# Performance work log

Hardware: AMD Instinct MI355X
Metric: run time of the kernel (lower is better)

Reference implementation:

```python
import jax, jax.numpy as jnp
import numpy as np

N_NODES = 50000
N_EDGES = 800000
D_IN = 64
F1 = 64
F2 = 64
D_HID = 100


def setup_inputs() -> dict:
    key = jax.random.key(0)
    ks = jax.random.split(key, 12)
    x = jax.random.normal(ks[0], (N_NODES, D_IN), dtype=jnp.float32)
    edge_src = jax.random.randint(ks[1], (N_EDGES,), 0, N_NODES, dtype=jnp.int32)
    edge_dst = jax.random.randint(ks[2], (N_EDGES,), 0, N_NODES, dtype=jnp.int32)
    # stands in for pre-normalized GCN adjacency values (D^-1/2 (A+I) D^-1/2)
    edge_weight = jax.random.uniform(ks[3], (N_EDGES,), dtype=jnp.float32)
    def glorot(k, shape):
        lim = np.sqrt(6.0 / (shape[0] + shape[1]))
        return jax.random.uniform(k, shape, jnp.float32, -lim, lim)
    W1 = glorot(ks[4], (D_IN, F1))
    b1 = jnp.zeros((F1,), jnp.float32)
    W2 = glorot(ks[5], (F1, F2))
    b2 = jnp.zeros((F2,), jnp.float32)
    Wd = glorot(ks[6], (F2, D_HID))
    bd = jnp.zeros((D_HID,), jnp.float32)
    Wo = glorot(ks[7], (D_HID, 1))
    bo = jnp.zeros((1,), jnp.float32)
    return {"x": x, "edge_src": edge_src, "edge_dst": edge_dst,
            "edge_weight": edge_weight, "W1": W1, "b1": b1, "W2": W2,
            "b2": b2, "Wd": Wd, "bd": bd, "Wo": Wo, "bo": bo}


def _gcn_conv(x, edge_src, edge_dst, edge_weight, W, b):
    # spektral GCNConv: out = swish(A_norm @ (X @ W) + b)
    h = x @ W                                        # [N, F]
    msg = h[edge_src] * edge_weight[:, None]          # [E, F] gather + scale
    agg = jax.ops.segment_sum(msg, edge_dst, num_segments=N_NODES)  # [N, F]
    return jax.nn.swish(agg + b)


def reference(x, edge_src, edge_dst, edge_weight, W1, b1, W2, b2, Wd, bd, Wo, bo):
    h = _gcn_conv(x, edge_src, edge_dst, edge_weight, W1, b1)
    h = _gcn_conv(h, edge_src, edge_dst, edge_weight, W2, b2)
    h = jax.nn.swish(h @ Wd + bd)                    # Dense(100, swish)
    return jax.nn.sigmoid(h @ Wo + bo)               # Dense(1, sigmoid) -> [N, 1]
```

## Files before the change

kernel.cpp:

```cpp
#include <hip/hip_runtime.h>
#include <hip/hip_fp16.h>

#define N_NODES 50000
#define N_EDGES 800000
#define D 64
#define DHID 100
#define NTILES (N_NODES / 16)
#define NCT 7
#define CAP 64
#define NGROUPS 8
#define NSLICES 390
#define FILL_BLOCKS (NGROUPS * NSLICES)
#define MM_BLOCKS ((NTILES + 3) / 4)
#define DST_PER_GROUP (N_NODES / NGROUPS)
#define FSTRIDE (NSLICES * 256)
#define KMAX 9

typedef unsigned short ushort;
typedef unsigned int uint;
typedef __attribute__((ext_vector_type(8))) short s16x8;
typedef __attribute__((ext_vector_type(4))) float f32x4;

#define MFMA16(A, B, C) __builtin_amdgcn_mfma_f32_16x16x32_bf16((A), (B), (C), 0, 0, 0)

__device__ __forceinline__ float swishf(float x) { return x / (1.0f + __expf(-x)); }

__device__ __forceinline__ ushort f2bf(float f) {
    uint u = __float_as_uint(f);
    uint r = (u + 0x7fffu + ((u >> 16) & 1u)) >> 16;
    return (ushort)r;
}
__device__ __forceinline__ float bf2f(ushort h) { return __uint_as_float((uint)h << 16); }
__device__ __forceinline__ float bf_lo(uint d) { return __uint_as_float(d << 16); }
__device__ __forceinline__ float bf_hi(uint d) { return __uint_as_float(d & 0xffff0000u); }

__device__ __forceinline__ float hwf(uint e) {
    return __half2float(__ushort_as_half((ushort)(e >> 16)));
}

__device__ __forceinline__ void accum8(float* acc, uint4 v, float w) {
    acc[0] = fmaf(w, bf_lo(v.x), acc[0]);
    acc[1] = fmaf(w, bf_hi(v.x), acc[1]);
    acc[2] = fmaf(w, bf_lo(v.y), acc[2]);
    acc[3] = fmaf(w, bf_hi(v.y), acc[3]);
    acc[4] = fmaf(w, bf_lo(v.z), acc[4]);
    acc[5] = fmaf(w, bf_hi(v.z), acc[5]);
    acc[6] = fmaf(w, bf_lo(v.w), acc[6]);
    acc[7] = fmaf(w, bf_hi(v.w), acc[7]);
}

__device__ __forceinline__ void gather_node2(const ushort* __restrict__ H,
                                             const uint* __restrict__ bucket,
                                             const int* __restrict__ degp,
                                             int j, int fg, float* acc) {
#pragma unroll
    for (int t = 0; t < 8; ++t) acc[t] = 0.f;
    const int sA = j * 4, sB = 16 + j * 4;
    uint4 eA = *((const uint4*)(bucket + sA));
    uint4 eB = *((const uint4*)(bucket + sB));
    int degv = min(*degp, CAP);

    bool pA = sA < degv, pB = sB < degv;
    uint4 vA0, vA1, vA2, vA3, vB0, vB1, vB2, vB3;
    float wA0 = 0, wA1 = 0, wA2 = 0, wA3 = 0;
    float wB0 = 0, wB1 = 0, wB2 = 0, wB3 = 0;
    if (pA) {
        wA0 = hwf(eA.x);
        wA1 = (sA + 1 < degv) ? hwf(eA.y) : 0.f;
        wA2 = (sA + 2 < degv) ? hwf(eA.z) : 0.f;
        wA3 = (sA + 3 < degv) ? hwf(eA.w) : 0.f;
        uint i0 = min(eA.x & 0xffffu, (uint)(N_NODES - 1));
        uint i1 = min(eA.y & 0xffffu, (uint)(N_NODES - 1));
        uint i2 = min(eA.z & 0xffffu, (uint)(N_NODES - 1));
        uint i3 = min(eA.w & 0xffffu, (uint)(N_NODES - 1));
        vA0 = *((const uint4*)(H + ((size_t)i0 << 6) + (fg << 3)));
        vA1 = *((const uint4*)(H + ((size_t)i1 << 6) + (fg << 3)));
        vA2 = *((const uint4*)(H + ((size_t)i2 << 6) + (fg << 3)));
        vA3 = *((const uint4*)(H + ((size_t)i3 << 6) + (fg << 3)));
    }
    if (pB) {
        wB0 = hwf(eB.x);
        wB1 = (sB + 1 < degv) ? hwf(eB.y) : 0.f;
        wB2 = (sB + 2 < degv) ? hwf(eB.z) : 0.f;
        wB3 = (sB + 3 < degv) ? hwf(eB.w) : 0.f;
        uint i0 = min(eB.x & 0xffffu, (uint)(N_NODES - 1));
        uint i1 = min(eB.y & 0xffffu, (uint)(N_NODES - 1));
        uint i2 = min(eB.z & 0xffffu, (uint)(N_NODES - 1));
        uint i3 = min(eB.w & 0xffffu, (uint)(N_NODES - 1));
        vB0 = *((const uint4*)(H + ((size_t)i0 << 6) + (fg << 3)));
        vB1 = *((const uint4*)(H + ((size_t)i1 << 6) + (fg << 3)));
        vB2 = *((const uint4*)(H + ((size_t)i2 << 6) + (fg << 3)));
        vB3 = *((const uint4*)(H + ((size_t)i3 << 6) + (fg << 3)));
    }
    if (pA) {
        accum8(acc, vA0, wA0);
        accum8(acc, vA1, wA1);
        accum8(acc, vA2, wA2);
        accum8(acc, vA3, wA3);
    }
    if (pB) {
        accum8(acc, vB0, wB0);
        accum8(acc, vB1, wB1);
        accum8(acc, vB2, wB2);
        accum8(acc, vB3, wB3);
    }
    for (int base = 32; base < degv; base += 16) {
        int s0 = base + j * 4;
        if (s0 < degv) {
            uint4 e = *((const uint4*)(bucket + s0));
            float w0 = hwf(e.x);
            float w1 = (s0 + 1 < degv) ? hwf(e.y) : 0.f;
            float w2 = (s0 + 2 < degv) ? hwf(e.z) : 0.f;
            float w3 = (s0 + 3 < degv) ? hwf(e.w) : 0.f;
            uint s0i = min(e.x & 0xffffu, (uint)(N_NODES - 1));
            uint s1i = min(e.y & 0xffffu, (uint)(N_NODES - 1));
            uint s2i = min(e.z & 0xffffu, (uint)(N_NODES - 1));
            uint s3i = min(e.w & 0xffffu, (uint)(N_NODES - 1));
            uint4 v0 = *((const uint4*)(H + ((size_t)s0i << 6) + (fg << 3)));
            uint4 v1 = *((const uint4*)(H + ((size_t)s1i << 6) + (fg << 3)));
            uint4 v2 = *((const uint4*)(H + ((size_t)s2i << 6) + (fg << 3)));
            uint4 v3 = *((const uint4*)(H + ((size_t)s3i << 6) + (fg << 3)));
            accum8(acc, v0, w0);
            accum8(acc, v1, w1);
            accum8(acc, v2, w2);
            accum8(acc, v3, w3);
        }
    }
#pragma unroll
    for (int t = 0; t < 8; ++t) {
        acc[t] += __shfl_xor(acc[t], 8, 64);
        acc[t] += __shfl_xor(acc[t], 16, 64);
    }
}

__global__ __launch_bounds__(256) void fill_and_l1(const int* __restrict__ src,
                                                   const int* __restrict__ dst,
                                                   const float* __restrict__ w,
                                                   int* __restrict__ deg,
                                                   uint* __restrict__ csr,
                                                   const float* __restrict__ X,
                                                   const float* __restrict__ W,
                                                   const float* __restrict__ W2,
                                                   const float* __restrict__ Wd,
                                                   short* __restrict__ W2T2,
                                                   short* __restrict__ WdT2,
                                                   ushort* __restrict__ H) {
    __shared__ __align__(16) short sBT[2][D][72];
    int tid = threadIdx.x;

    if (blockIdx.x < FILL_BLOCKS) {
        const int g = blockIdx.x & (NGROUPS - 1);
        const int s = blockIdx.x >> 3;
        const int lo = g * DST_PER_GROUP;
        const int e0 = s * 256 + tid;
        int d[KMAX];
        bool mk[KMAX];
#pragma unroll
        for (int k = 0; k < KMAX; ++k) {
            int e = e0 + k * FSTRIDE;
            int dv = (e < N_EDGES) ? __builtin_nontemporal_load(dst + e) : -1;
            d[k] = dv;
            mk[k] = ((uint)(dv - lo) < (uint)DST_PER_GROUP);
        }
        float wv9[KMAX];
        int sv9[KMAX];
#pragma unroll
        for (int k = 0; k < KMAX; ++k)
            if (mk[k]) {
                int e = e0 + k * FSTRIDE;
                wv9[k] = __builtin_nontemporal_load(w + e);
                sv9[k] = __builtin_nontemporal_load(src + e);
            }
        int r9[KMAX];
#pragma unroll
        for (int k = 0; k < KMAX; ++k)
            if (mk[k]) r9[k] = atomicAdd(&deg[d[k]], 1);
#pragma unroll
        for (int k = 0; k < KMAX; ++k)
            if (mk[k]) {
                uint hw = (uint)__half_as_ushort(__float2half_rn(wv9[k]));
                uint payload = (uint)sv9[k] | (hw << 16);
                int r = min(r9[k], CAP - 1);
                csr[(d[k] << 6) + r] = payload;
            }
        return;
    }

    if (blockIdx.x >= FILL_BLOCKS + MM_BLOCKS) {
        if (blockIdx.x == FILL_BLOCKS + MM_BLOCKS) {
            for (int idx = tid; idx < D * D; idx += 256) {
                int k = idx >> 6, c = idx & 63;
                float wv = W2[idx];
                ushort hi = f2bf(wv);
                W2T2[(size_t)c * D + k] = (short)hi;
                W2T2[(size_t)(D + c) * D + k] = (short)f2bf(wv - bf2f(hi));
            }
        } else {
            for (int idx = tid; idx < NCT * 16 * D; idx += 256) {
                int jj = idx >> 6, k = idx & 63;
                float wv = (jj < DHID) ? Wd[k * DHID + jj] : 0.f;
                ushort hi = f2bf(wv);
                WdT2[(size_t)jj * D + k] = (short)hi;
                WdT2[(size_t)(NCT * 16 + jj) * D + k] = (short)f2bf(wv - bf2f(hi));
            }
        }
        return;
    }

    for (int idx = tid; idx < D * D; idx += 256) {
        int k = idx >> 6, c = idx & 63;
        float wv = W[idx];
        ushort hi = f2bf(wv);
        sBT[0][c][k] = (short)hi;
        sBT[1][c][k] = (short)f2bf(wv - bf2f(hi));
    }
    __syncthreads();
    int wv_ = tid >> 6, lane = tid & 63, quad = lane >> 4, m = lane & 15;
    int tile = min((blockIdx.x - FILL_BLOCKS) * 4 + wv_, NTILES - 1);
    int node0 = tile * 16;

    f32x4 acc[4] = {{0,0,0,0},{0,0,0,0},{0,0,0,0},{0,0,0,0}};
#pragma unroll
    for (int kt = 0; kt < 2; ++kt) {
        int k0 = kt * 32 + quad * 8;
        const float* xp = X + ((size_t)(node0 + m) << 6) + k0;
        f32x4 xa = __builtin_nontemporal_load((const f32x4*)xp);
        f32x4 xb = __builtin_nontemporal_load((const f32x4*)(xp + 4));
        float xv[8] = {xa[0], xa[1], xa[2], xa[3], xb[0], xb[1], xb[2], xb[3]};
        s16x8 ahi, alo;
#pragma unroll
        for (int jj = 0; jj < 8; ++jj) {
            ushort hi = f2bf(xv[jj]);
            ahi[jj] = (short)hi;
            alo[jj] = (short)f2bf(xv[jj] - bf2f(hi));
        }
#pragma unroll
        for (int ct = 0; ct < 4; ++ct) {
            int n = ct * 16 + m;
            s16x8 bhi = *((const s16x8*)&sBT[0][n][k0]);
            s16x8 blo = *((const s16x8*)&sBT[1][n][k0]);
            acc[ct] = MFMA16(ahi, bhi, acc[ct]);
            acc[ct] = MFMA16(ahi, blo, acc[ct]);
            acc[ct] = MFMA16(alo, bhi, acc[ct]);
        }
    }
    __syncthreads();
    short (*rep)[16][72] = (short(*)[16][72])&sBT[0][0][0];
#pragma unroll
    for (int ct = 0; ct < 4; ++ct)
#pragma unroll
        for (int r = 0; r < 4; ++r)
            rep[wv_][quad * 4 + r][ct * 16 + m] = (short)f2bf(acc[ct][r]);
#pragma unroll
    for (int half = 0; half < 2; ++half) {
        int r = (lane >> 3) + half * 8;
        int c0 = (lane & 7) * 8;
        s16x8 v = *((const s16x8*)&rep[wv_][r][c0]);
        *((s16x8*)(H + ((size_t)(node0 + r) << 6) + c0)) = v;
    }
}

__global__ __launch_bounds__(256) void gather_act(const ushort* __restrict__ H,
                                                  const int* __restrict__ deg,
                                                  const uint* __restrict__ csr,
                                                  const float* __restrict__ bias,
                                                  ushort* __restrict__ actOut) {
    int tid = threadIdx.x;
    int wave = tid >> 6, lane = tid & 63;
    int h = lane >> 5, j = (lane >> 3) & 3, fg = lane & 7;
    int node = blockIdx.x * 8 + wave * 2 + h;
    const uint* bucket = csr + ((size_t)node << 6);

    float acc[8];
    gather_node2(H, bucket, deg + node, j, fg, acc);
    if (j == 0) {
        float4 ba = ((const float4*)bias)[fg * 2];
        float4 bb = ((const float4*)bias)[fg * 2 + 1];
        float r0 = swishf(acc[0] + ba.x);
        float r1 = swishf(acc[1] + ba.y);
        float r2 = swishf(acc[2] + ba.z);
        float r3 = swishf(acc[3] + ba.w);
        float r4 = swishf(acc[4] + bb.x);
        float r5 = swishf(acc[5] + bb.y);
        float r6 = swishf(acc[6] + bb.z);
        float r7 = swishf(acc[7] + bb.w);
        uint4 u;
        u.x = (uint)f2bf(r0) | ((uint)f2bf(r1) << 16);
        u.y = (uint)f2bf(r2) | ((uint)f2bf(r3) << 16);
        u.z = (uint)f2bf(r4) | ((uint)f2bf(r5) << 16);
        u.w = (uint)f2bf(r6) | ((uint)f2bf(r7) << 16);
        *((uint4*)(actOut + ((size_t)node << 6) + (fg << 3))) = u;
    }
}

__global__ __launch_bounds__(512) void gather_tail(const ushort* __restrict__ act1,
                                                   const int* __restrict__ deg,
                                                   const uint* __restrict__ csr,
                                                   const short* __restrict__ W2T2,
                                                   const float* __restrict__ b2,
                                                   const short* __restrict__ WdT2,
                                                   const float* __restrict__ bd,
                                                   const float* __restrict__ Wo,
                                                   const float* __restrict__ bo,
                                                   float* __restrict__ out) {
    __shared__ __align__(16) float sAgg[16][72];
    __shared__ __align__(16) short sAct2[16][72];
    __shared__ float sPart[8][16];
    int tid = threadIdx.x;
    int wv = tid >> 6, lane = tid & 63;
    int h = lane >> 5, j = (lane >> 3) & 3, fg = lane & 7;
    int quad = lane >> 4, m = lane & 15;
    int node0 = blockIdx.x * 16;

    {
        int nl = wv * 2 + h;
        int node = node0 + nl;
        const uint* bucket = csr + ((size_t)node << 6);
        float acc[8];
        gather_node2(act1, bucket, deg + node, j, fg, acc);
        if (j == 0) {
            float4 u0 = {acc[0], acc[1], acc[2], acc[3]};
            float4 u1 = {acc[4], acc[5], acc[6], acc[7]};
            *((float4*)&sAgg[nl][fg * 8]) = u0;
            *((float4*)&sAgg[nl][fg * 8 + 4]) = u1;
        }
    }
    __syncthreads();

    if (wv < 4) {
        f32x4 acc = {0, 0, 0, 0};
        int n = wv * 16 + m;
#pragma unroll
        for (int kt = 0; kt < 2; ++kt) {
            int k0 = kt * 32 + quad * 8;
            float4 xa = *((const float4*)&sAgg[m][k0]);
            float4 xb = *((const float4*)&sAgg[m][k0 + 4]);
            float xv[8] = {xa.x, xa.y, xa.z, xa.w, xb.x, xb.y, xb.z, xb.w};
            s16x8 ahi, alo;
#pragma unroll
            for (int jj = 0; jj < 8; ++jj) {
                ushort hi = f2bf(xv[jj]);
                ahi[jj] = (short)hi;
                alo[jj] = (short)f2bf(xv[jj] - bf2f(hi));
            }
            s16x8 bhi = *((const s16x8*)(W2T2 + (size_t)n * D + k0));
            s16x8 blo = *((const s16x8*)(W2T2 + (size_t)(D + n) * D + k0));
            acc = MFMA16(ahi, bhi, acc);
            acc = MFMA16(ahi, blo, acc);
            acc = MFMA16(alo, bhi, acc);
        }
        float bv = b2[n];
#pragma unroll
        for (int r = 0; r < 4; ++r)
            sAct2[quad * 4 + r][n] = (short)f2bf(swishf(acc[r] + bv));
    }
    __syncthreads();

    float part[4] = {0, 0, 0, 0};
    if (wv < NCT) {
        f32x4 acc = {0, 0, 0, 0};
        int n = wv * 16 + m;
#pragma unroll
        for (int kt = 0; kt < 2; ++kt) {
            int k0 = kt * 32 + quad * 8;
            s16x8 a = *((const s16x8*)&sAct2[m][k0]);
            s16x8 bhi = *((const s16x8*)(WdT2 + (size_t)n * D + k0));
            s16x8 blo = *((const s16x8*)(WdT2 + (size_t)(NCT * 16 + n) * D + k0));
            acc = MFMA16(a, bhi, acc);
            acc = MFMA16(a, blo, acc);
        }
        float bdv = (n < DHID) ? bd[n] : 0.f;
        float wov = (n < DHID) ? Wo[n] : 0.f;
#pragma unroll
        for (int r = 0; r < 4; ++r)
            part[r] = fmaf(swishf(acc[r] + bdv), wov, part[r]);
    }
#pragma unroll
    for (int r = 0; r < 4; ++r) {
        part[r] += __shfl_xor(part[r], 1, 64);
        part[r] += __shfl_xor(part[r], 2, 64);
        part[r] += __shfl_xor(part[r], 4, 64);
        part[r] += __shfl_xor(part[r], 8, 64);
    }
    if (m == 0) {
#pragma unroll
        for (int r = 0; r < 4; ++r)
            sPart[wv][quad * 4 + r] = part[r];
    }
    __syncthreads();
    if (tid < 16) {
        float z = bo[0];
#pragma unroll
        for (int i = 0; i < 8; ++i) z += sPart[i][tid];
        out[node0 + tid] = 1.f / (1.f + __expf(-z));
    }
}

extern "C" void kernel_launch(void* const* d_in, const int* in_sizes, int n_in,
                              void* d_out, int out_size, void* d_ws, size_t ws_size,
                              hipStream_t stream) {
    const float* x   = (const float*)d_in[0];
    const int* esrc  = (const int*)d_in[1];
    const int* edst  = (const int*)d_in[2];
    const float* ew  = (const float*)d_in[3];
    const float* W1  = (const float*)d_in[4];
    const float* b1  = (const float*)d_in[5];
    const float* W2  = (const float*)d_in[6];
    const float* b2  = (const float*)d_in[7];
    const float* Wd  = (const float*)d_in[8];
    const float* bd  = (const float*)d_in[9];
    const float* Wo  = (const float*)d_in[10];
    const float* bo  = (const float*)d_in[11];
    float* out = (float*)d_out;

    char* ws = (char*)d_ws;
    ushort* H1   = (ushort*)ws;  ws += (size_t)N_NODES * D * sizeof(ushort);
    ushort* act1 = (ushort*)ws;  ws += (size_t)N_NODES * D * sizeof(ushort);
    uint* csr    = (uint*)ws;    ws += (size_t)N_NODES * CAP * sizeof(uint);
    int* deg     = (int*)ws;     ws += (size_t)N_NODES * sizeof(int);
    short* W2T2  = (short*)ws;   ws += (size_t)2 * D * D * sizeof(short);
    short* WdT2  = (short*)ws;   ws += (size_t)2 * NCT * 16 * D * sizeof(short);

    const int gBlocks = N_NODES / 8;

    hipMemsetAsync(deg, 0, (size_t)N_NODES * sizeof(int), stream);

    fill_and_l1<<<FILL_BLOCKS + MM_BLOCKS + 2, 256, 0, stream>>>(
        esrc, edst, ew, deg, csr, x, W1, W2, Wd, W2T2, WdT2, H1);

    gather_act<<<gBlocks, 256, 0, stream>>>(H1, deg, csr, b1, act1);

    gather_tail<<<NTILES, 512, 0, stream>>>(act1, deg, csr, W2T2, b2, WdT2, bd, Wo, bo, out);
}
```

Baseline: 195.4 us.

## Halve fill destination groups, drop nontemporal loads, shrink gather_tail blocks

The CSR fill now splits destinations into 4 groups instead of 8, so each edge array is read 4 times instead of 8, with more slices and 5 edges per thread. Nontemporal loads are replaced by normal cached loads for edge arrays and X. gather_tail moves from 512 to 256 threads per block, so each wave gathers two node pairs and handles up to two dense column tiles. Together these aim to cut redundant edge reads and idle waves, at the cost of more atomic contention per group and more serial work per wave.

After: 182.1 us. 1.07x faster.

```diff
diff --git a/kernel.cpp b/kernel.cpp
--- a/kernel.cpp
+++ b/kernel.cpp
@@ -8,13 +8,13 @@
 #define NTILES (N_NODES / 16)
 #define NCT 7
 #define CAP 64
-#define NGROUPS 8
-#define NSLICES 390
+#define NGROUPS 4
+#define NSLICES 780
 #define FILL_BLOCKS (NGROUPS * NSLICES)
 #define MM_BLOCKS ((NTILES + 3) / 4)
 #define DST_PER_GROUP (N_NODES / NGROUPS)
 #define FSTRIDE (NSLICES * 256)
-#define KMAX 9
+#define KMAX 5
 
 typedef unsigned short ushort;
 typedef unsigned int uint;
@@ -150,7 +150,7 @@
 
     if (blockIdx.x < FILL_BLOCKS) {
         const int g = blockIdx.x & (NGROUPS - 1);
-        const int s = blockIdx.x >> 3;
+        const int s = blockIdx.x >> 2;
         const int lo = g * DST_PER_GROUP;
         const int e0 = s * 256 + tid;
         int d[KMAX];
@@ -158,29 +158,29 @@
 #pragma unroll
         for (int k = 0; k < KMAX; ++k) {
             int e = e0 + k * FSTRIDE;
-            int dv = (e < N_EDGES) ? __builtin_nontemporal_load(dst + e) : -1;
+            int dv = (e < N_EDGES) ? dst[e] : -1;
             d[k] = dv;
             mk[k] = ((uint)(dv - lo) < (uint)DST_PER_GROUP);
         }
-        float wv9[KMAX];
-        int sv9[KMAX];
+        float wv5[KMAX];
+        int sv5[KMAX];
 #pragma unroll
         for (int k = 0; k < KMAX; ++k)
             if (mk[k]) {
                 int e = e0 + k * FSTRIDE;
-                wv9[k] = __builtin_nontemporal_load(w + e);
-                sv9[k] = __builtin_nontemporal_load(src + e);
-            }
-        int r9[KMAX];
+                wv5[k] = w[e];
+                sv5[k] = src[e];
+            }
+        int r5[KMAX];
 #pragma unroll
         for (int k = 0; k < KMAX; ++k)
-            if (mk[k]) r9[k] = atomicAdd(&deg[d[k]], 1);
+            if (mk[k]) r5[k] = atomicAdd(&deg[d[k]], 1);
 #pragma unroll
         for (int k = 0; k < KMAX; ++k)
             if (mk[k]) {
-                uint hw = (uint)__half_as_ushort(__float2half_rn(wv9[k]));
-                uint payload = (uint)sv9[k] | (hw << 16);
-                int r = min(r9[k], CAP - 1);
+                uint hw = (uint)__half_as_ushort(__float2half_rn(wv5[k]));
+                uint payload = (uint)sv5[k] | (hw << 16);
+                int r = min(r5[k], CAP - 1);
                 csr[(d[k] << 6) + r] = payload;
             }
         return;
@@ -224,9 +224,9 @@
     for (int kt = 0; kt < 2; ++kt) {
         int k0 = kt * 32 + quad * 8;
         const float* xp = X + ((size_t)(node0 + m) << 6) + k0;
-        f32x4 xa = __builtin_nontemporal_load((const f32x4*)xp);
-        f32x4 xb = __builtin_nontemporal_load((const f32x4*)(xp + 4));
-        float xv[8] = {xa[0], xa[1], xa[2], xa[3], xb[0], xb[1], xb[2], xb[3]};
+        float4 xa = *((const float4*)xp);
+        float4 xb = *((const float4*)(xp + 4));
+        float xv[8] = {xa.x, xa.y, xa.z, xa.w, xb.x, xb.y, xb.z, xb.w};
         s16x8 ahi, alo;
 #pragma unroll
         for (int jj = 0; jj < 8; ++jj) {
@@ -293,7 +293,7 @@
     }
 }
 
-__global__ __launch_bounds__(512) void gather_tail(const ushort* __restrict__ act1,
+__global__ __launch_bounds__(256) void gather_tail(const ushort* __restrict__ act1,
                                                    const int* __restrict__ deg,
                                                    const uint* __restrict__ csr,
                                                    const short* __restrict__ W2T2,
@@ -305,15 +305,15 @@
                                                    float* __restrict__ out) {
     __shared__ __align__(16) float sAgg[16][72];
     __shared__ __align__(16) short sAct2[16][72];
-    __shared__ float sPart[8][16];
+    __shared__ float sPart[4][16];
     int tid = threadIdx.x;
     int wv = tid >> 6, lane = tid & 63;
     int h = lane >> 5, j = (lane >> 3) & 3, fg = lane & 7;
     int quad = lane >> 4, m = lane & 15;
     int node0 = blockIdx.x * 16;
 
-    {
-        int nl = wv * 2 + h;
+    for (int t = 0; t < 2; ++t) {
+        int nl = wv * 4 + t * 2 + h;
         int node = node0 + nl;
         const uint* bucket = csr + ((size_t)node << 6);
         float acc[8];
@@ -327,7 +327,7 @@
     }
     __syncthreads();
 
-    if (wv < 4) {
+    {
         f32x4 acc = {0, 0, 0, 0};
         int n = wv * 16 + m;
 #pragma unroll
@@ -357,23 +357,27 @@
     __syncthreads();
 
     float part[4] = {0, 0, 0, 0};
-    if (wv < NCT) {
-        f32x4 acc = {0, 0, 0, 0};
-        int n = wv * 16 + m;
-#pragma unroll
-        for (int kt = 0; kt < 2; ++kt) {
-            int k0 = kt * 32 + quad * 8;
-            s16x8 a = *((const s16x8*)&sAct2[m][k0]);
-            s16x8 bhi = *((const s16x8*)(WdT2 + (size_t)n * D + k0));
-            s16x8 blo = *((const s16x8*)(WdT2 + (size_t)(NCT * 16 + n) * D + k0));
-            acc = MFMA16(a, bhi, acc);
-            acc = MFMA16(a, blo, acc);
-        }
-        float bdv = (n < DHID) ? bd[n] : 0.f;
-        float wov = (n < DHID) ? Wo[n] : 0.f;
-#pragma unroll
-        for (int r = 0; r < 4; ++r)
-            part[r] = fmaf(swishf(acc[r] + bdv), wov, part[r]);
+#pragma unroll
+    for (int cc = 0; cc < 2; ++cc) {
+        int ct = wv + cc * 4;
+        if (ct < NCT) {
+            f32x4 acc = {0, 0, 0, 0};
+            int n = ct * 16 + m;
+#pragma unroll
+            for (int kt = 0; kt < 2; ++kt) {
+                int k0 = kt * 32 + quad * 8;
+                s16x8 a = *((const s16x8*)&sAct2[m][k0]);
+                s16x8 bhi = *((const s16x8*)(WdT2 + (size_t)n * D + k0));
+                s16x8 blo = *((const s16x8*)(WdT2 + (size_t)(NCT * 16 + n) * D + k0));
+                acc = MFMA16(a, bhi, acc);
+                acc = MFMA16(a, blo, acc);
+            }
+            float bdv = (n < DHID) ? bd[n] : 0.f;
+            float wov = (n < DHID) ? Wo[n] : 0.f;
+#pragma unroll
+            for (int r = 0; r < 4; ++r)
+                part[r] = fmaf(swishf(acc[r] + bdv), wov, part[r]);
+        }
     }
 #pragma unroll
     for (int r = 0; r < 4; ++r) {
@@ -389,10 +393,8 @@
     }
     __syncthreads();
     if (tid < 16) {
-        float z = bo[0];
-#pragma unroll
-        for (int i = 0; i < 8; ++i) z += sPart[i][tid];
-        out[node0 + tid] = 1.f / (1.f + __expf(-z));
+        float z = sPart[0][tid] + sPart[1][tid] + sPart[2][tid] + sPart[3][tid] + bo[0];
+        out[blockIdx.x * 16 + tid] = 1.f / (1.f + __expf(-z));
     }
 }
 
@@ -430,5 +432,5 @@
 
     gather_act<<<gBlocks, 256, 0, stream>>>(H1, deg, csr, b1, act1);
 
-    gather_tail<<<NTILES, 512, 0, stream>>>(act1, deg, csr, W2T2, b2, WdT2, bd, Wo, bo, out);
-}
+    gather_tail<<<NTILES, 256, 0, stream>>>(act1, deg, csr, W2T2, b2, WdT2, bd, Wo, bo, out);
+}
```
